# Kernel tuning notes

Hardware: AMD Instinct MI355X
Metric: run time of the kernel (lower is better)

The kernel has to match this reference:

```python
import jax, jax.numpy as jnp
import numpy as np
from jax import lax

STRIDES = (8, 16, 32)
REG_MAX = 16
NUM_CLASSES = 80
CLS_OUT = NUM_CLASSES + 1  # 81
REG_OUT = 4 * (REG_MAX + 1)  # 68
IN_CH = (128, 256, 512)
FEAT_HW = ((80, 80), (40, 40), (20, 20))
BATCH = 32


def _conv3(x, w, b):
    # x: [N,C,H,W], w: [O,C,3,3] -> SAME padding, stride 1
    y = lax.conv_general_dilated(x, w, (1, 1), 'SAME',
                                 dimension_numbers=('NCHW', 'OIHW', 'NCHW'))
    return y + b[None, :, None, None]


def _level_priors(h, w, stride):
    # matches get_single_level_center_priors: x fastest-varying
    xs = jnp.arange(w, dtype=jnp.float32) * stride
    ys = jnp.arange(h, dtype=jnp.float32) * stride
    x = jnp.tile(xs[None, :], (h, 1)).reshape(-1)
    y = jnp.tile(ys[:, None], (1, w)).reshape(-1)
    s = jnp.full((h * w,), float(stride), dtype=jnp.float32)
    return jnp.stack([x, y, s, s], axis=-1)  # [HW,4]


def setup_inputs() -> dict:
    key = jax.random.key(0)
    ks = jax.random.split(key, 16)
    d = {}
    for i, (c, (h, w)) in enumerate(zip(IN_CH, FEAT_HW)):
        d[f'x{i}'] = jax.random.normal(ks[i], (BATCH, c, h, w), dtype=jnp.float32)
    ki = 3
    for i, c in enumerate(IN_CH):
        d[f'wc{i}'] = jax.random.normal(ks[ki], (CLS_OUT, c, 3, 3), dtype=jnp.float32) * 0.02; ki += 1
        d[f'bc{i}'] = jnp.full((CLS_OUT,), -4.595, dtype=jnp.float32)  # bias_init_with_prob(0.01)
        d[f'wr{i}'] = jax.random.normal(ks[ki], (REG_OUT, c, 3, 3), dtype=jnp.float32) * 0.02; ki += 1
        d[f'br{i}'] = jnp.zeros((REG_OUT,), dtype=jnp.float32)
    d['scales'] = jnp.ones((3,), dtype=jnp.float32)
    return d


def reference(x0, x1, x2, wc0, bc0, wr0, br0, wc1, bc1, wr1, br1,
              wc2, bc2, wr2, br2, scales):
    xs = (x0, x1, x2)
    wcs, bcs = (wc0, wc1, wc2), (bc0, bc1, bc2)
    wrs, brs = (wr0, wr1, wr2), (br0, br1, br2)
    cls_list, box_list, prior_list = [], [], []
    for i in range(3):
        x = xs[i]
        N, _, H, W = x.shape
        # forward_single (stacked_convs=0 -> no tower convs)
        bbox = _conv3(x, wrs[i], brs[i]) * scales[i]          # [N,68,H,W]
        bbox = bbox.reshape(N, 4, REG_MAX + 1, H, W)
        bbox = jax.nn.softmax(bbox, axis=2)                   # softmax over bins
        bbox = bbox.reshape(N, 4, REG_MAX + 1, H * W).transpose(0, 3, 1, 2)  # [N,HW,4,17]
        cls = jax.nn.sigmoid(_conv3(x, wcs[i], bcs[i]))       # [N,81,H,W]
        cls = cls.reshape(N, CLS_OUT, H * W).transpose(0, 2, 1)  # [N,HW,81]
        cls_list.append(cls)
        box_list.append(bbox)
        prior_list.append(_level_priors(H, W, STRIDES[i]))
    cls_scores = jnp.concatenate(cls_list, axis=1)[:, :, :NUM_CLASSES]  # [N,A,80]
    bbox_dist = jnp.concatenate(box_list, axis=1)                        # [N,A,4,17]
    priors = jnp.concatenate(prior_list, axis=0)[None]                   # [1,A,4]
    # Integral: expectation over bins 0..reg_max
    project = jnp.arange(REG_MAX + 1, dtype=bbox_dist.dtype)
    dist = jnp.einsum('nafr,r->naf', bbox_dist, project)                 # [N,A,4]
    dist = dist * priors[..., 2, None]                                   # scale by stride
    # distance2bbox
    px, py = priors[..., 0], priors[..., 1]
    bboxes = jnp.stack([px - dist[..., 0], py - dist[..., 1],
                        px + dist[..., 2], py + dist[..., 3]], axis=-1)  # [N,A,4]
    return cls_scores, bboxes
```

## Files before the change

### kernel.cpp

```cpp
#include <hip/hip_runtime.h>
#include <hip/hip_bf16.h>
#include <math.h>

#define BATCH   32
#define A_TOTAL 8400
#define NCLS    80

typedef __attribute__((ext_vector_type(8))) short bf16x8;
typedef __attribute__((ext_vector_type(4))) float f32x4;

__device__ __forceinline__ short f2bf(float f) {
    union { float f; unsigned u; } v; v.f = f;
    unsigned u = v.u + 0x7fffu + ((v.u >> 16) & 1u);
    return (short)(u >> 16);
}

__device__ __forceinline__ float fsig(float x) {
    return __builtin_amdgcn_rcpf(1.f + __expf(-x));
}

__device__ __forceinline__ void stage16(const void* g, void* ldsp) {
    __builtin_amdgcn_global_load_lds(
        (const __attribute__((address_space(1))) unsigned int*)g,
        (__attribute__((address_space(3))) unsigned int*)ldsp, 16, 0, 0);
}

__device__ __forceinline__ void prep_w_body(const float* wc, const float* wr,
                                            __hip_bfloat16* af, int C, int bidl) {
    const int KC = C / 32;
    const int total = 9 * KC * 10 * 64;
    int idx = bidl * 256 + threadIdx.x;
    if (idx >= total) return;
    int l   = idx & 63;
    int rem = idx >> 6;
    int mf  = rem % 10;
    int kc  = (rem / 10) % KC;
    int tap = rem / (10 * KC);
    int m     = mf * 16 + (l & 15);
    int cbase = kc * 32 + (l >> 4) * 8;
    short v[8];
#pragma unroll
    for (int j = 0; j < 8; ++j) {
        int c = cbase + j;
        float w = 0.f;
        if (m < 80)        w = wc[((size_t)m * C + c) * 9 + tap];
        else if (m < 148)  w = wr[((size_t)(m - 80) * C + c) * 9 + tap];
        v[j] = f2bf(w);
    }
    *(bf16x8*)((short*)af + (size_t)idx * 8) = *(bf16x8*)v;
}

__global__ __launch_bounds__(256) void prep_w_all(
    const float* __restrict__ wc0, const float* __restrict__ wr0,
    const float* __restrict__ wc1, const float* __restrict__ wr1,
    const float* __restrict__ wc2, const float* __restrict__ wr2,
    __hip_bfloat16* __restrict__ af0, __hip_bfloat16* __restrict__ af1,
    __hip_bfloat16* __restrict__ af2) {
    int b = blockIdx.x;
    if (b < 90)       prep_w_body(wc0, wr0, af0, 128, b);
    else if (b < 270) prep_w_body(wc1, wr1, af1, 256, b - 90);
    else              prep_w_body(wc2, wr2, af2, 512, b - 270);
}

template<int C, int H, int W>
__global__ __launch_bounds__(256) void transpose_x(const float* __restrict__ x,
                                                   __hip_bfloat16* __restrict__ xT) {
    const int CC  = C / 64;
    const int KC  = C / 32;
    const int PW  = W + 2;
    const int PHW = (H + 2) * PW;
    int b   = blockIdx.x;
    int cch = b % CC;
    int y   = (b / CC) % H;
    int n   = b / (CC * H);
    __shared__ float sm[64][W + 1];
    const float* src = x + (((size_t)n * C + cch * 64) * H + y) * W;
    for (int i = threadIdx.x; i < 64 * (W / 4); i += 256) {
        int c = i / (W / 4), f4 = i % (W / 4);
        float4 v = *(const float4*)(src + (size_t)c * H * W + f4 * 4);
        sm[c][f4 * 4 + 0] = v.x;
        sm[c][f4 * 4 + 1] = v.y;
        sm[c][f4 * 4 + 2] = v.z;
        sm[c][f4 * 4 + 3] = v.w;
    }
    __syncthreads();
    short* base = (short*)xT + (size_t)n * KC * 4 * PHW * 8;
    for (int u = threadIdx.x; u < W * 8; u += 256) {
        int g8 = u / W, xc = u % W;
        int kc = cch * 2 + (g8 >> 2);
        int j  = g8 & 3;
        short v[8];
#pragma unroll
        for (int jj = 0; jj < 8; ++jj) v[jj] = f2bf(sm[g8 * 8 + jj][xc]);
        *(bf16x8*)(base + (((size_t)(kc * 4 + j)) * PHW + (y + 1) * PW + xc + 1) * 8) =
            *(bf16x8*)v;
    }
    bf16x8 z = (bf16x8)(short)0;
    if (threadIdx.x < 16) {
        int g8 = threadIdx.x >> 1, side = threadIdx.x & 1;
        int kc = cch * 2 + (g8 >> 2), j = g8 & 3;
        *(bf16x8*)(base + (((size_t)(kc * 4 + j)) * PHW + (y + 1) * PW + side * (W + 1)) * 8) = z;
    }
    if (y == 0) {
        for (int u = threadIdx.x; u < PW * 8; u += 256) {
            int g8 = u / PW, col = u % PW;
            int kc = cch * 2 + (g8 >> 2), j = g8 & 3;
            *(bf16x8*)(base + (((size_t)(kc * 4 + j)) * PHW + col) * 8) = z;
        }
    }
    if (y == H - 1) {
        for (int u = threadIdx.x; u < PW * 8; u += 256) {
            int g8 = u / PW, col = u % PW;
            int kc = cch * 2 + (g8 >> 2), j = g8 & 3;
            *(bf16x8*)(base + (((size_t)(kc * 4 + j)) * PHW + (H + 1) * PW + col) * 8) = z;
        }
    }
}

template<int C, int H, int W, int STRIDE, int A_OFFp, int LVL, int NT, int KS,
         int NTHR, int WEU>
__global__ __launch_bounds__(NTHR, WEU) void gemm_head(
    const __hip_bfloat16* __restrict__ xT,
    const __hip_bfloat16* __restrict__ af,
    const float* __restrict__ bc, const float* __restrict__ br,
    const float* __restrict__ scales,
    float* __restrict__ out_cls, float* __restrict__ out_box,
    float* __restrict__ pbuf) {
    constexpr int HW     = H * W;
    constexpr int PW     = W + 2;
    constexpr int PHW    = (H + 2) * PW;
    constexpr int WAVES  = NTHR / 64;
    constexpr int WN     = WAVES / 2;
    constexpr int NF     = NT / (16 * WN);
    static_assert(NT == WN * NF * 16, "NT must equal WN*NF*16");
    constexpr int TILES  = (HW + NT - 1) / NT;
    constexpr int KC     = C / 32;
    constexpr int KCS    = KC / KS;
    constexpr int DYMAX  = (NT - 1) / W + 1;
    constexpr int NSTAGE = NT + 2 * DYMAX + 2 * W + 7;
    constexpr int NS16   = NSTAGE * 16;
    constexpr int NG     = NSTAGE * 4;
    constexpr int ITB    = (NG + NTHR - 1) / NTHR;
    constexpr int BSZ    = ITB * NTHR * 16;
    constexpr int EPI    = 68 * (NT + 4) * 4;
    constexpr int LDSB   = (KS > 1) ? (2 * BSZ) : ((2 * BSZ) > EPI ? (2 * BSZ) : EPI);
    static_assert(ITB <= 9, "B staging spread exceeds tap steps");

    __shared__ __align__(16) char lds[LDSB];

    constexpr int NWG = BATCH * TILES * KS;
    const int bid  = blockIdx.x;
    const int swz  = (bid & 7) * (NWG / 8) + (bid >> 3);
    const int ks   = swz % KS;
    const int rest = swz / KS;
    const int tile = rest % TILES;
    const int n    = rest / TILES;

    const int tid   = threadIdx.x;
    const int l     = tid & 63;
    const int wid   = __builtin_amdgcn_readfirstlane(tid >> 6);
    const int mhalf = wid & 1;
    const int ng    = wid >> 1;
    const int lr    = l & 15;
    const int kg    = l >> 4;

    const char* xb  = (const char*)xT + (size_t)n * KC * 4 * PHW * 16;
    const char* afc = (const char*)af;

    const int p0    = tile * NT;
    const int qbase = (p0 / W) * PW + (p0 % W);

    int blane[NF];
#pragma unroll
    for (int nf = 0; nf < NF; ++nf) {
        int p  = p0 + (ng * NF + nf) * 16 + lr;
        int qc = (p / W + 1) * PW + (p % W) + 1;
        blane[nf] = kg * NS16 + (qc - (W + 3) - qbase) * 16;
    }

    unsigned bsoff[ITB];
#pragma unroll
    for (int it = 0; it < ITB; ++it) {
        int idx = it * NTHR + tid;
        int j = idx / NSTAGE; if (j > 3) j = 3;
        int q = qbase + (idx - j * NSTAGE);
        if (q > PHW - 1) q = PHW - 1;
        bsoff[it] = (unsigned)((j * PHW + q) * 16);
    }

    f32x4 acc[5][NF];
#pragma unroll
    for (int mf = 0; mf < 5; ++mf)
#pragma unroll
        for (int nf = 0; nf < NF; ++nf) acc[mf][nf] = (f32x4)0.f;

    auto stageB = [&](int it, int kc, unsigned dstbase) {
        stage16(xb + (size_t)kc * (4 * PHW * 16) + bsoff[it],
                &lds[dstbase + it * (NTHR * 16) + wid * 1024]);
    };
    auto loadA = [&](bf16x8* dst, int step) {
        const char* asrc = afc + (size_t)step * 10240 + mhalf * 5120 + l * 16;
#pragma unroll
        for (int mf = 0; mf < 5; ++mf)
            dst[mf] = *(const bf16x8*)(asrc + mf * 1024);
    };

    const int kc0 = ks * KCS;

    bf16x8 acur[5], anxt[5];
    loadA(acur, kc0);

#pragma unroll
    for (int it = 0; it < ITB; ++it) stageB(it, kc0, 0);
    __syncthreads();

    unsigned curB = 0;

#pragma unroll 1
    for (int kk = 0; kk < KCS; ++kk) {
        const int kc = kc0 + kk;
#pragma unroll
        for (int tap = 0; tap < 9; ++tap) {
            if (tap < ITB && kk + 1 < KCS)
                stageB(tap, kc + 1, curB ^ BSZ);
            const int nstep = (tap == 8) ? (kc + 1) : ((tap + 1) * KC + kc);
            loadA(anxt, nstep);
            const int imm = ((tap / 3) * PW + (tap % 3)) * 16;
            __builtin_amdgcn_s_setprio(1);
#pragma unroll
            for (int nf = 0; nf < NF; ++nf) {
                bf16x8 b = *(const bf16x8*)&lds[curB + blane[nf] + imm];
#pragma unroll
                for (int mf = 0; mf < 5; ++mf)
                    acc[mf][nf] = __builtin_amdgcn_mfma_f32_16x16x32_bf16(
                        acur[mf], b, acc[mf][nf], 0, 0, 0);
            }
            __builtin_amdgcn_s_setprio(0);
#pragma unroll
            for (int mf = 0; mf < 5; ++mf) acur[mf] = anxt[mf];
        }
        __syncthreads();
        curB ^= BSZ;
    }

    if constexpr (KS > 1) {
        float* pb = pbuf + (size_t)((n * TILES + tile) * KS + ks) * (160 * NT);
#pragma unroll
        for (int mf = 0; mf < 5; ++mf)
#pragma unroll
            for (int nf = 0; nf < NF; ++nf) {
                int col = (ng * NF + nf) * 16 + lr;
#pragma unroll
                for (int r = 0; r < 4; ++r) {
                    int ch = mhalf * 80 + mf * 16 + kg * 4 + r;
                    pb[ch * NT + col] = acc[mf][nf][r];
                }
            }
        return;
    } else {
        const float sc = scales[LVL];
        float* smf = (float*)lds;

        if (mhalf == 0) {
            float4 bias[5];
#pragma unroll
            for (int mf = 0; mf < 5; ++mf)
                bias[mf] = *(const float4*)(bc + mf * 16 + kg * 4);
#pragma unroll
            for (int nf = 0; nf < NF; ++nf) {
                int p = p0 + (ng * NF + nf) * 16 + lr;
                if (p < HW) {
                    float* oc = out_cls + ((size_t)n * A_TOTAL + A_OFFp + p) * NCLS;
#pragma unroll
                    for (int mf = 0; mf < 5; ++mf) {
                        f32x4 v = acc[mf][nf];
                        float4 s;
                        s.x = fsig(v[0] + bias[mf].x);
                        s.y = fsig(v[1] + bias[mf].y);
                        s.z = fsig(v[2] + bias[mf].z);
                        s.w = fsig(v[3] + bias[mf].w);
                        *(float4*)(oc + mf * 16 + kg * 4) = s;
                    }
                }
            }
        } else {
#pragma unroll
            for (int mf = 0; mf < 5; ++mf)
#pragma unroll
                for (int nf = 0; nf < NF; ++nf) {
                    int lpx = (ng * NF + nf) * 16 + lr;
#pragma unroll
                    for (int r = 0; r < 4; ++r) {
                        int ch = mf * 16 + kg * 4 + r;
                        if (ch < 68) smf[ch * (NT + 4) + lpx] = acc[mf][nf][r];
                    }
                }
        }
        __syncthreads();

        for (int u = tid; u < 4 * NT; u += NTHR) {
            int f   = u / NT;
            int lpx = u % NT;
            int p   = p0 + lpx;
            if (p < HW) {
                float lg[17];
                float m = -1e30f;
#pragma unroll
                for (int r = 0; r < 17; ++r) {
                    lg[r] = (smf[(f * 17 + r) * (NT + 4) + lpx] + br[f * 17 + r]) * sc;
                    m = fmaxf(m, lg[r]);
                }
                float ssum = 0.f, esum = 0.f;
#pragma unroll
                for (int r = 0; r < 17; ++r) {
                    float e = __expf(lg[r] - m);
                    ssum += e;
                    esum += e * (float)r;
                }
                const float dist = esum * __builtin_amdgcn_rcpf(ssum) * (float)STRIDE;
                const int py = p / W, px = p % W;
                const float base = (f & 1) ? (float)(py * STRIDE) : (float)(px * STRIDE);
                const float val  = (f < 2) ? (base - dist) : (base + dist);
                out_box[((size_t)n * A_TOTAL + A_OFFp + p) * 4 + f] = val;
            }
        }
    }
}

template<int H, int W, int STRIDE, int A_OFFp, int LVL, int TILES, int KS>
__global__ __launch_bounds__(256) void reduce_epi(
    const float* __restrict__ pbuf,
    const float* __restrict__ bc, const float* __restrict__ br,
    const float* __restrict__ scales,
    float* __restrict__ out_cls, float* __restrict__ out_box) {
    constexpr int HW = H * W;
    const int bid  = blockIdx.x;
    const int tile = bid % TILES;
    const int n    = bid / TILES;
    const int tid  = threadIdx.x;
    const float* pb = pbuf + (size_t)(n * TILES + tile) * KS * 10240;

    __shared__ float smf[160 * 66];
    for (int idx = tid; idx < 160 * 64; idx += 256) {
        float s = 0.f;
#pragma unroll
        for (int k = 0; k < KS; ++k) s += pb[k * 10240 + idx];
        smf[(idx >> 6) * 66 + (idx & 63)] = s;
    }
    __syncthreads();

    const int q = tid >> 6;
    const int t = tid & 63;
    const int p = tile * 64 + t;
    if (p < HW) {
        float* oc = out_cls + ((size_t)n * A_TOTAL + A_OFFp + p) * NCLS + q * 20;
#pragma unroll
        for (int k = 0; k < 20; k += 4) {
            float4 v;
            v.x = fsig(smf[(q * 20 + k + 0) * 66 + t] + bc[q * 20 + k + 0]);
            v.y = fsig(smf[(q * 20 + k + 1) * 66 + t] + bc[q * 20 + k + 1]);
            v.z = fsig(smf[(q * 20 + k + 2) * 66 + t] + bc[q * 20 + k + 2]);
            v.w = fsig(smf[(q * 20 + k + 3) * 66 + t] + bc[q * 20 + k + 3]);
            *(float4*)(oc + k) = v;
        }
        const float sc = scales[LVL];
        float lg[17];
        float m = -1e30f;
#pragma unroll
        for (int r = 0; r < 17; ++r) {
            lg[r] = (smf[(80 + q * 17 + r) * 66 + t] + br[q * 17 + r]) * sc;
            m = fmaxf(m, lg[r]);
        }
        float ssum = 0.f, esum = 0.f;
#pragma unroll
        for (int r = 0; r < 17; ++r) {
            float e = __expf(lg[r] - m);
            ssum += e;
            esum += e * (float)r;
        }
        const float dist = esum * __builtin_amdgcn_rcpf(ssum) * (float)STRIDE;
        const int py = p / W, px = p % W;
        const float base = (q & 1) ? (float)(py * STRIDE) : (float)(px * STRIDE);
        const float val  = (q < 2) ? (base - dist) : (base + dist);
        out_box[((size_t)n * A_TOTAL + A_OFFp + p) * 4 + q] = val;
    }
}

extern "C" void kernel_launch(void* const* d_in, const int* in_sizes, int n_in,
                              void* d_out, int out_size, void* d_ws, size_t ws_size,
                              hipStream_t stream) {
    const float* x0  = (const float*)d_in[0];
    const float* x1  = (const float*)d_in[1];
    const float* x2  = (const float*)d_in[2];
    const float* wc0 = (const float*)d_in[3];
    const float* bc0 = (const float*)d_in[4];
    const float* wr0 = (const float*)d_in[5];
    const float* br0 = (const float*)d_in[6];
    const float* wc1 = (const float*)d_in[7];
    const float* bc1 = (const float*)d_in[8];
    const float* wr1 = (const float*)d_in[9];
    const float* br1 = (const float*)d_in[10];
    const float* wc2 = (const float*)d_in[11];
    const float* bc2 = (const float*)d_in[12];
    const float* wr2 = (const float*)d_in[13];
    const float* br2 = (const float*)d_in[14];
    const float* scl = (const float*)d_in[15];

    float* out_cls = (float*)d_out;
    float* out_box = (float*)d_out + (size_t)BATCH * A_TOTAL * NCLS;

    __hip_bfloat16* af  = (__hip_bfloat16*)d_ws;
    __hip_bfloat16* af0 = af;
    __hip_bfloat16* af1 = af + 184320;
    __hip_bfloat16* af2 = af + 552960;
    __hip_bfloat16* xT  = af + 1290240;
    float* pbuf = (float*)((char*)xT + 15859712);

    prep_w_all<<<dim3(630), 256, 0, stream>>>(wc0, wr0, wc1, wr1, wc2, wr2,
                                              af0, af1, af2);

    transpose_x<128, 80, 80><<<dim3(32 * 80 * 2), 256, 0, stream>>>(x0, xT);
    gemm_head<128, 80, 80, 8, 0, 0, 96, 1, 256, 3><<<dim3(32 * 67), 256, 0, stream>>>(
        xT, af0, bc0, br0, scl, out_cls, out_box, nullptr);

    transpose_x<256, 40, 40><<<dim3(32 * 40 * 4), 256, 0, stream>>>(x1, xT);
    gemm_head<256, 40, 40, 16, 6400, 1, 128, 1, 512, 4><<<dim3(32 * 13), 512, 0, stream>>>(
        xT, af1, bc1, br1, scl, out_cls, out_box, nullptr);

    transpose_x<512, 20, 20><<<dim3(32 * 20 * 8), 256, 0, stream>>>(x2, xT);
    gemm_head<512, 20, 20, 32, 8000, 2, 64, 4, 256, 4><<<dim3(32 * 7 * 4), 256, 0, stream>>>(
        xT, af2, bc2, br2, scl, out_cls, out_box, pbuf);
    reduce_epi<20, 20, 32, 8000, 2, 7, 4><<<dim3(32 * 7), 256, 0, stream>>>(
        pbuf, bc2, br2, scl, out_cls, out_box);
}
```

Measured before the change: 252.2 us.

## Reuse LDS B-fragments across horizontal taps via DPP lane shifts for level 0

For the 80x80 level, the conv-GEMM now uses a 2-row, 160-pixel tile. Each of the three kernel rows loads its B fragments from LDS once, and the left and right taps are built by shifting those fragments across lanes with DPP row-shift operations. This removes two thirds of the LDS reads for B. In exchange the tile and grid shapes change (fewer, larger workgroups, occupancy hint lowered from 3 to 2 waves per EU), the per-dy staging layout changes, and extra DPP VALU instructions are added.

```diff
diff --git a/kernel.cpp b/kernel.cpp
--- a/kernel.cpp
+++ b/kernel.cpp
@@ -23,6 +23,25 @@
     __builtin_amdgcn_global_load_lds(
         (const __attribute__((address_space(1))) unsigned int*)g,
         (__attribute__((address_space(3))) unsigned int*)ldsp, 16, 0, 0);
+}
+
+__device__ __forceinline__ bf16x8 shp1(bf16x8 cur, bf16x8 nxt) {
+    union { bf16x8 v; int d[4]; } c{cur}, n{nxt}, r;
+#pragma unroll
+    for (int i = 0; i < 4; ++i) {
+        int t = __builtin_amdgcn_update_dpp(0, n.d[i], 0x11F, 0xF, 0xF, false);
+        r.d[i] = __builtin_amdgcn_update_dpp(t, c.d[i], 0x101, 0xF, 0xF, false);
+    }
+    return r.v;
+}
+__device__ __forceinline__ bf16x8 shm1(bf16x8 cur, bf16x8 prv) {
+    union { bf16x8 v; int d[4]; } c{cur}, p{prv}, r;
+#pragma unroll
+    for (int i = 0; i < 4; ++i) {
+        int t = __builtin_amdgcn_update_dpp(0, p.d[i], 0x10F, 0xF, 0xF, false);
+        r.d[i] = __builtin_amdgcn_update_dpp(t, c.d[i], 0x111, 0xF, 0xF, false);
+    }
+    return r.v;
 }
 
 __device__ __forceinline__ void prep_w_body(const float* wc, const float* wr,
@@ -118,7 +137,7 @@
 }
 
 template<int C, int H, int W, int STRIDE, int A_OFFp, int LVL, int NT, int KS,
-         int NTHR, int WEU>
+         int NTHR, int WEU, int DPPB>
 __global__ __launch_bounds__(NTHR, WEU) void gemm_head(
     const __hip_bfloat16* __restrict__ xT,
     const __hip_bfloat16* __restrict__ af,
@@ -133,6 +152,8 @@
     constexpr int WN     = WAVES / 2;
     constexpr int NF     = NT / (16 * WN);
     static_assert(NT == WN * NF * 16, "NT must equal WN*NF*16");
+    static_assert(!DPPB || (NF == 5 && W == 80 && NT == 160 && NTHR == 256 && KS == 1),
+                  "DPP path assumes 2-row 160px tile");
     constexpr int TILES  = (HW + NT - 1) / NT;
     constexpr int KC     = C / 32;
     constexpr int KCS    = KC / KS;
@@ -140,11 +161,11 @@
     constexpr int NSTAGE = NT + 2 * DYMAX + 2 * W + 7;
     constexpr int NS16   = NSTAGE * 16;
     constexpr int NG     = NSTAGE * 4;
-    constexpr int ITB    = (NG + NTHR - 1) / NTHR;
-    constexpr int BSZ    = ITB * NTHR * 16;
+    constexpr int ITBv   = DPPB ? 9 : ((NG + NTHR - 1) / NTHR);
+    constexpr int BSZ    = DPPB ? (9 * NTHR * 16) : (ITBv * NTHR * 16);
     constexpr int EPI    = 68 * (NT + 4) * 4;
     constexpr int LDSB   = (KS > 1) ? (2 * BSZ) : ((2 * BSZ) > EPI ? (2 * BSZ) : EPI);
-    static_assert(ITB <= 9, "B staging spread exceeds tap steps");
+    static_assert(ITBv <= 9, "B staging spread exceeds tap steps");
 
     __shared__ __align__(16) char lds[LDSB];
 
@@ -168,24 +189,38 @@
     const char* afc = (const char*)af;
 
     const int p0    = tile * NT;
-    const int qbase = (p0 / W) * PW + (p0 % W);
 
     int blane[NF];
-#pragma unroll
-    for (int nf = 0; nf < NF; ++nf) {
-        int p  = p0 + (ng * NF + nf) * 16 + lr;
-        int qc = (p / W + 1) * PW + (p % W) + 1;
-        blane[nf] = kg * NS16 + (qc - (W + 3) - qbase) * 16;
-    }
-
-    unsigned bsoff[ITB];
-#pragma unroll
-    for (int it = 0; it < ITB; ++it) {
-        int idx = it * NTHR + tid;
-        int j = idx / NSTAGE; if (j > 3) j = 3;
-        int q = qbase + (idx - j * NSTAGE);
-        if (q > PHW - 1) q = PHW - 1;
-        bsoff[it] = (unsigned)((j * PHW + q) * 16);
+    unsigned bsoff[ITBv];
+    int base2 = 0;
+    if constexpr (DPPB) {
+        base2 = (kg * 515 + lr + 1) * 16;
+#pragma unroll
+        for (int it = 0; it < ITBv; ++it) {
+            int idx = it * NTHR + tid; if (idx > 2059) idx = 2059;
+            int j = idx / 515;
+            int rem = idx - j * 515; if (rem > 511) rem = 511;
+            int g = rem >> 7, px = rem & 127;
+            int pos = px - 16; pos = pos < 0 ? 0 : (pos > W + 1 ? W + 1 : pos);
+            int q = (2 * tile + g) * PW + pos;
+            bsoff[it] = (unsigned)((j * PHW + q) * 16);
+        }
+    } else {
+        const int qbase = (p0 / W) * PW + (p0 % W);
+#pragma unroll
+        for (int nf = 0; nf < NF; ++nf) {
+            int p  = p0 + (ng * NF + nf) * 16 + lr;
+            int qc = (p / W + 1) * PW + (p % W) + 1;
+            blane[nf] = kg * NS16 + (qc - (W + 3) - qbase) * 16;
+        }
+#pragma unroll
+        for (int it = 0; it < ITBv; ++it) {
+            int idx = it * NTHR + tid;
+            int j = idx / NSTAGE; if (j > 3) j = 3;
+            int q = qbase + (idx - j * NSTAGE);
+            if (q > PHW - 1) q = PHW - 1;
+            bsoff[it] = (unsigned)((j * PHW + q) * 16);
+        }
     }
 
     f32x4 acc[5][NF];
@@ -211,36 +246,82 @@
     loadA(acur, kc0);
 
 #pragma unroll
-    for (int it = 0; it < ITB; ++it) stageB(it, kc0, 0);
+    for (int it = 0; it < ITBv; ++it) stageB(it, kc0, 0);
     __syncthreads();
 
     unsigned curB = 0;
 
-#pragma unroll 1
-    for (int kk = 0; kk < KCS; ++kk) {
-        const int kc = kc0 + kk;
-#pragma unroll
-        for (int tap = 0; tap < 9; ++tap) {
-            if (tap < ITB && kk + 1 < KCS)
-                stageB(tap, kc + 1, curB ^ BSZ);
+    if constexpr (DPPB) {
+        auto doTap = [&](int tap, int kc, bf16x8 b0, bf16x8 b1, bf16x8 b2,
+                         bf16x8 b3, bf16x8 b4) {
             const int nstep = (tap == 8) ? (kc + 1) : ((tap + 1) * KC + kc);
             loadA(anxt, nstep);
-            const int imm = ((tap / 3) * PW + (tap % 3)) * 16;
+            bf16x8 bv[5] = {b0, b1, b2, b3, b4};
             __builtin_amdgcn_s_setprio(1);
 #pragma unroll
-            for (int nf = 0; nf < NF; ++nf) {
-                bf16x8 b = *(const bf16x8*)&lds[curB + blane[nf] + imm];
+            for (int nf = 0; nf < 5; ++nf)
 #pragma unroll
                 for (int mf = 0; mf < 5; ++mf)
                     acc[mf][nf] = __builtin_amdgcn_mfma_f32_16x16x32_bf16(
-                        acur[mf], b, acc[mf][nf], 0, 0, 0);
+                        acur[mf], bv[nf], acc[mf][nf], 0, 0, 0);
+            __builtin_amdgcn_s_setprio(0);
+#pragma unroll
+            for (int mf = 0; mf < 5; ++mf) acur[mf] = anxt[mf];
+        };
+#pragma unroll 1
+        for (int kk = 0; kk < KCS; ++kk) {
+            const int kc = kc0 + kk;
+#pragma unroll
+            for (int dy = 0; dy < 3; ++dy) {
+                if (kk + 1 < KCS) {
+#pragma unroll
+                    for (int it = dy * 3; it < dy * 3 + 3; ++it)
+                        stageB(it, kc + 1, BSZ - curB);
+                }
+                const int dyi = curB + base2 + (ng + dy) * 2048;
+                bf16x8 fm = *(const bf16x8*)&lds[dyi];
+                bf16x8 f0 = *(const bf16x8*)&lds[dyi + 256];
+                bf16x8 f1 = *(const bf16x8*)&lds[dyi + 512];
+                bf16x8 f2 = *(const bf16x8*)&lds[dyi + 768];
+                bf16x8 f3 = *(const bf16x8*)&lds[dyi + 1024];
+                bf16x8 f4 = *(const bf16x8*)&lds[dyi + 1280];
+                bf16x8 fp = *(const bf16x8*)&lds[dyi + 1536];
+                doTap(dy * 3 + 0, kc, shm1(f0, fm), shm1(f1, f0), shm1(f2, f1),
+                      shm1(f3, f2), shm1(f4, f3));
+                doTap(dy * 3 + 1, kc, f0, f1, f2, f3, f4);
+                doTap(dy * 3 + 2, kc, shp1(f0, f1), shp1(f1, f2), shp1(f2, f3),
+                      shp1(f3, f4), shp1(f4, fp));
             }
-            __builtin_amdgcn_s_setprio(0);
-#pragma unroll
-            for (int mf = 0; mf < 5; ++mf) acur[mf] = anxt[mf];
-        }
-        __syncthreads();
-        curB ^= BSZ;
+            __syncthreads();
+            curB = BSZ - curB;
+        }
+    } else {
+#pragma unroll 1
+        for (int kk = 0; kk < KCS; ++kk) {
+            const int kc = kc0 + kk;
+#pragma unroll
+            for (int tap = 0; tap < 9; ++tap) {
+                if (tap < ITBv && kk + 1 < KCS)
+                    stageB(tap, kc + 1, curB ^ BSZ);
+                const int nstep = (tap == 8) ? (kc + 1) : ((tap + 1) * KC + kc);
+                loadA(anxt, nstep);
+                const int imm = ((tap / 3) * PW + (tap % 3)) * 16;
+                __builtin_amdgcn_s_setprio(1);
+#pragma unroll
+                for (int nf = 0; nf < NF; ++nf) {
+                    bf16x8 b = *(const bf16x8*)&lds[curB + blane[nf] + imm];
+#pragma unroll
+                    for (int mf = 0; mf < 5; ++mf)
+                        acc[mf][nf] = __builtin_amdgcn_mfma_f32_16x16x32_bf16(
+                            acur[mf], b, acc[mf][nf], 0, 0, 0);
+                }
+                __builtin_amdgcn_s_setprio(0);
+#pragma unroll
+                for (int mf = 0; mf < 5; ++mf) acur[mf] = anxt[mf];
+            }
+            __syncthreads();
+            curB ^= BSZ;
+        }
     }
 
     if constexpr (KS > 1) {
@@ -420,15 +501,15 @@
                                               af0, af1, af2);
 
     transpose_x<128, 80, 80><<<dim3(32 * 80 * 2), 256, 0, stream>>>(x0, xT);
-    gemm_head<128, 80, 80, 8, 0, 0, 96, 1, 256, 3><<<dim3(32 * 67), 256, 0, stream>>>(
+    gemm_head<128, 80, 80, 8, 0, 0, 160, 1, 256, 2, 1><<<dim3(32 * 40), 256, 0, stream>>>(
         xT, af0, bc0, br0, scl, out_cls, out_box, nullptr);
 
     transpose_x<256, 40, 40><<<dim3(32 * 40 * 4), 256, 0, stream>>>(x1, xT);
-    gemm_head<256, 40, 40, 16, 6400, 1, 128, 1, 512, 4><<<dim3(32 * 13), 512, 0, stream>>>(
+    gemm_head<256, 40, 40, 16, 6400, 1, 128, 1, 512, 4, 0><<<dim3(32 * 13), 512, 0, stream>>>(
         xT, af1, bc1, br1, scl, out_cls, out_box, nullptr);
 
     transpose_x<512, 20, 20><<<dim3(32 * 20 * 8), 256, 0, stream>>>(x2, xT);
-    gemm_head<512, 20, 20, 32, 8000, 2, 64, 4, 256, 4><<<dim3(32 * 7 * 4), 256, 0, stream>>>(
+    gemm_head<512, 20, 20, 32, 8000, 2, 64, 4, 256, 4, 0><<<dim3(32 * 7 * 4), 256, 0, stream>>>(
         xT, af2, bc2, br2, scl, out_cls, out_box, pbuf);
     reduce_epi<20, 20, 32, 8000, 2, 7, 4><<<dim3(32 * 7), 256, 0, stream>>>(
         pbuf, bc2, br2, scl, out_cls, out_box);
```

Result: faster. 241.5 us (-4.2%).
